# Kernel tuning notes

Measured on AMD Instinct MI355X. Metric: run time of the kernel, lower is better.

## Reference

```python
import jax, jax.numpy as jnp
import numpy as np
from jax import lax

B, T, BYTE_LEN, EMB = 8, 4096, 8, 64
FILTERS = [(1, 4), (2, 8), (3, 12), (4, 16), (5, 20), (6, 24), (7, 28)]
LAST_DIM = sum(c for _, c in FILTERS)  # 112
OUT_DIM = 512


def setup_inputs() -> dict:
    key = jax.random.key(0)
    ks = jax.random.split(key, 32)
    inp = {"features": jax.random.normal(ks[0], (B, T, BYTE_LEN, EMB), dtype=jnp.float32)}
    for i, (w, c) in enumerate(FILTERS):
        inp[f"conv_w{i+1}"] = jax.random.normal(ks[1 + i], (c, EMB, w), dtype=jnp.float32) * 0.05
        inp[f"conv_b{i+1}"] = jax.random.normal(ks[8 + i], (c,), dtype=jnp.float32) * 0.05
    inp["hw_w1"] = jax.random.normal(ks[15], (2 * LAST_DIM, LAST_DIM), dtype=jnp.float32) * 0.05
    inp["hw_b1"] = jnp.concatenate([jnp.zeros(LAST_DIM), jnp.ones(LAST_DIM)]).astype(jnp.float32)
    inp["hw_w2"] = jax.random.normal(ks[16], (2 * LAST_DIM, LAST_DIM), dtype=jnp.float32) * 0.05
    inp["hw_b2"] = jnp.concatenate([jnp.zeros(LAST_DIM), jnp.ones(LAST_DIM)]).astype(jnp.float32)
    inp["proj_w"] = jax.random.normal(ks[17], (OUT_DIM, LAST_DIM), dtype=jnp.float32) * 0.05
    inp["proj_b"] = jax.random.normal(ks[18], (OUT_DIM,), dtype=jnp.float32) * 0.05
    return inp


def _conv_branch(x, w, b):
    # x: [N, EMB, BYTE_LEN], w: [out_c, EMB, width] -> max over time, relu -> [N, out_c]
    y = lax.conv_general_dilated(x, w, window_strides=(1,), padding='VALID',
                                 dimension_numbers=('NCH', 'OIH', 'NCH'))
    y = y + b[None, :, None]
    return jax.nn.relu(jnp.max(y, axis=-1))


def _highway_layer(x, w, b):
    p = x @ w.T + b
    proj_x, gate = jnp.split(p, 2, axis=-1)
    g = jax.nn.sigmoid(gate)
    return g * x + (1.0 - g) * jax.nn.relu(proj_x)


def reference(features, conv_w1, conv_w2, conv_w3, conv_w4, conv_w5, conv_w6, conv_w7,
              conv_b1, conv_b2, conv_b3, conv_b4, conv_b5, conv_b6, conv_b7,
              hw_w1, hw_b1, hw_w2, hw_b2, proj_w, proj_b):
    b, t, byte_len, emb = features.shape
    # transpose(2,3).view(-1, emb, byte_len)
    x = features.transpose(0, 1, 3, 2).reshape(-1, emb, byte_len)  # [B*T, EMB, BYTE_LEN]
    ws = [conv_w1, conv_w2, conv_w3, conv_w4, conv_w5, conv_w6, conv_w7]
    bs = [conv_b1, conv_b2, conv_b3, conv_b4, conv_b5, conv_b6, conv_b7]
    branches = [_conv_branch(x, w, bb) for w, bb in zip(ws, bs)]
    h = jnp.concatenate(branches, axis=-1)  # [B*T, LAST_DIM]
    h = _highway_layer(h, hw_w1, hw_b1)
    h = _highway_layer(h, hw_w2, hw_b2)
    out = h @ proj_w.T + proj_b  # [B*T, OUT_DIM]
    return out.reshape(b, t, -1)
```

## Files before the change

### kernel.cpp

```cpp
#include <hip/hip_runtime.h>

typedef __attribute__((ext_vector_type(8))) short short8;
typedef __attribute__((ext_vector_type(4))) float f32x4;

#define KDIM 512
#define NCT  30
#define BCHUNK 32768

__device__ __forceinline__ unsigned short f2bf(float x) {
    unsigned u = __float_as_uint(x);
    return (unsigned short)((u + 0x7FFFu + ((u >> 16) & 1u)) >> 16);
}
__device__ __forceinline__ float bf2f(unsigned short h) {
    return __uint_as_float(((unsigned)h) << 16);
}

__device__ __forceinline__ void stage16(const void* g, void* l, int lane) {
    __builtin_amdgcn_global_load_lds(
        (const __attribute__((address_space(1))) unsigned int*)g,
        (__attribute__((address_space(3))) unsigned int*)l, 16, 0, 0);
}

__global__ __launch_bounds__(256) void prep_kernel(
        const float* __restrict__ w1, const float* __restrict__ w2,
        const float* __restrict__ w3, const float* __restrict__ w4,
        const float* __restrict__ w5, const float* __restrict__ w6,
        const float* __restrict__ w7, const float* __restrict__ hw1,
        const float* __restrict__ hw2, const float* __restrict__ pw,
        unsigned short* __restrict__ WC, unsigned short* __restrict__ W1s,
        unsigned short* __restrict__ W2s, unsigned short* __restrict__ Ps) {
    int gid = blockIdx.x * 256 + threadIdx.x;
    if (gid < 30720) {
        int kb = gid / 480, col = gid % 480;
        const float* wp; int cbnd, NP, C, W;
        if (col < 32)       { wp = w1; cbnd = 0;   NP = 8; C = 4;  W = 1; }
        else if (col < 96)  { wp = w2; cbnd = 32;  NP = 7; C = 8;  W = 2; }
        else if (col < 176) { wp = w3; cbnd = 96;  NP = 6; C = 12; W = 3; }
        else if (col < 256) { wp = w4; cbnd = 176; NP = 5; C = 16; W = 4; }
        else if (col < 336) { wp = w5; cbnd = 256; NP = 4; C = 20; W = 5; }
        else if (col < 416) { wp = w6; cbnd = 336; NP = 3; C = 24; W = 6; }
        else                { wp = w7; cbnd = 416; NP = 2; C = 28; W = 7; }
        int c2 = col - cbnd, oc = c2 / NP, p = c2 - oc * NP;
        int j = kb >> 3, dk = j - p, e0 = (kb & 7) * 8;
        bool valid = (oc < C) && (dk >= 0) && (dk < W);
        short8 v8;
#pragma unroll
        for (int i = 0; i < 8; ++i) {
            float v = valid ? wp[(oc * 64 + e0 + i) * W + dk] : 0.f;
            v8[i] = (short)f2bf(v);
        }
        int q = kb >> 2, krh = kb & 3;
        *(short8*)(WC + (size_t)q * 16384 + ((col >> 4) * 64 + krh * 16 + (col & 15)) * 8) = v8;
    } else if (gid < 30720 + 7168) {
        int x = gid - 30720;
        const float* src = (x < 3584) ? hw1 : hw2;
        unsigned short* dst = (x < 3584) ? W1s : W2s;
        if (x >= 3584) x -= 3584;
        int kb = x / 224, n = x % 224, k0 = kb * 8;
        short8 v8;
#pragma unroll
        for (int i = 0; i < 8; ++i) {
            float v = (k0 + i < 112) ? src[n * 112 + k0 + i] : 0.f;
            v8[i] = (short)f2bf(v);
        }
        int q = kb >> 2, krh = kb & 3;
        *(short8*)(dst + q * 8192 + ((n >> 4) * 64 + krh * 16 + (n & 15)) * 8) = v8;
    } else if (gid < 30720 + 7168 + 8192) {
        int x = gid - 37888;
        int kb = x / 512, n = x % 512, k0 = kb * 8;
        short8 v8;
#pragma unroll
        for (int i = 0; i < 8; ++i) {
            float v = (k0 + i < 112) ? pw[n * 112 + k0 + i] : 0.f;
            v8[i] = (short)f2bf(v);
        }
        int q = kb >> 2, krh = kb & 3;
        *(short8*)(Ps + ((q * 32 + (n >> 4)) * 64 + krh * 16 + (n & 15)) * 8) = v8;
    }
}

template <int T0, int NT>
__device__ __forceinline__ void dump_phase(float* Cb, const f32x4* acc, int wave, int lane) {
    int r0 = wave * 16 + ((lane >> 4) * 4);
    int c0 = lane & 15;
#pragma unroll
    for (int tt = 0; tt < NT; ++tt)
#pragma unroll
        for (int r = 0; r < 4; ++r)
            Cb[(r0 + r) * 161 + tt * 16 + c0] = acc[T0 + tt][r];
}

__device__ void reduce_phase(const float* Cb, unsigned short* ht, int tid,
                             int cA, int NPA, int choffA, int colbA, const float* cbA,
                             int cB, int NPB, int choffB, int colbB, const float* cbB) {
    int noc = cA + cB;
    for (int idx = tid; idx < 64 * noc; idx += 256) {
        int row = idx & 63, ocp = idx >> 6;
        bool isB = ocp >= cA;
        int oc = isB ? ocp - cA : ocp;
        int NP = isB ? NPB : NPA;
        int colb = isB ? colbB : colbA;
        int choff = isB ? choffB : choffA;
        const float* cb = isB ? cbB : cbA;
        const float* src = Cb + row * 161 + colb + oc * NP;
        float m = src[0];
        for (int k = 1; k < NP; ++k) m = fmaxf(m, src[k]);
        float v = fmaxf(m + cb[oc], 0.f);
        ht[row * 136 + choff + oc] = f2bf(v);
    }
}

__global__ __launch_bounds__(256, 2) void fused_kernel(
        const float* __restrict__ feat, const unsigned short* __restrict__ WC,
        const float* cb0, const float* cb1, const float* cb2, const float* cb3,
        const float* cb4, const float* cb5, const float* cb6,
        const unsigned short* __restrict__ W1, const unsigned short* __restrict__ W2,
        const unsigned short* __restrict__ PW,
        const float* __restrict__ hb1, const float* __restrict__ hb2,
        const float* __restrict__ pb, float* __restrict__ out) {
    __shared__ __align__(16) char sm[65536];
    const int tid = threadIdx.x, lane = tid & 63, wave = tid >> 6;
    const int c0 = lane & 15, kq = lane >> 4;
    const int m0 = blockIdx.x * 64;
    f32x4 zero = {0.f, 0.f, 0.f, 0.f};

    const float* arow = feat + (size_t)(m0 + wave * 16 + c0) * KDIM + kq * 8;
    short8 af[16];
#pragma unroll
    for (int q = 0; q < 16; ++q) {
        float t[8];
        *(float4*)(t)     = *(const float4*)(arow + q * 32);
        *(float4*)(t + 4) = *(const float4*)(arow + q * 32 + 4);
        short8 v;
#pragma unroll
        for (int i = 0; i < 8; ++i) v[i] = (short)f2bf(t[i]);
        af[q] = v;
    }

    f32x4 acc[NCT];
#pragma unroll
    for (int t = 0; t < NCT; ++t) acc[t] = zero;

    for (int i = tid; i < 2048; i += 256)
        stage16(WC + i * 8, sm + (i - lane) * 16, lane);

#pragma unroll
    for (int q = 0; q < 16; ++q) {
        if (q < 15) {
            const unsigned short* src = WC + (q + 1) * 16384;
            char* dst = sm + ((q + 1) & 1) * BCHUNK;
            for (int i = tid; i < 2048; i += 256)
                stage16(src + i * 8, dst + (i - lane) * 16, lane);
            asm volatile("s_waitcnt vmcnt(8)" ::: "memory");
        } else {
            asm volatile("s_waitcnt vmcnt(0)" ::: "memory");
        }
        __builtin_amdgcn_s_barrier();
        const char* bb = sm + (q & 1) * BCHUNK;
        __builtin_amdgcn_s_setprio(1);
#pragma unroll
        for (int t = 0; t < NCT; ++t) {
            short8 b = *(const short8*)(bb + (t * 64 + lane) * 16);
            acc[t] = __builtin_amdgcn_mfma_f32_16x16x32_bf16(af[q], b, acc[t], 0, 0, 0);
        }
        __builtin_amdgcn_s_setprio(0);
        asm volatile("s_waitcnt lgkmcnt(0)" ::: "memory");
        __builtin_amdgcn_s_barrier();
    }

    float* Cb = (float*)sm;
    unsigned short* ht = (unsigned short*)(sm + 41216);
    __syncthreads();
    for (int i = tid; i < 1024; i += 256)
        ht[(i >> 4) * 136 + 112 + (i & 15)] = 0;
    dump_phase<0, 6>(Cb, acc, wave, lane);
    __syncthreads();
    reduce_phase(Cb, ht, tid, 4, 8, 0, 0, cb0, 8, 7, 4, 32, cb1);
    __syncthreads();
    dump_phase<6, 10>(Cb, acc, wave, lane);
    __syncthreads();
    reduce_phase(Cb, ht, tid, 12, 6, 12, 0, cb2, 16, 5, 24, 80, cb3);
    __syncthreads();
    dump_phase<16, 10>(Cb, acc, wave, lane);
    __syncthreads();
    reduce_phase(Cb, ht, tid, 20, 4, 40, 0, cb4, 24, 3, 60, 80, cb5);
    __syncthreads();
    dump_phase<26, 4>(Cb, acc, wave, lane);
    __syncthreads();
    reduce_phase(Cb, ht, tid, 28, 2, 84, 0, cb6, 0, 1, 0, 0, cb6);
    __syncthreads();

    char* wb = sm;
    short8 a2[4];
#pragma unroll
    for (int q = 0; q < 4; ++q)
        a2[q] = *(const short8*)((const char*)ht + (wave * 16 + c0) * 272 + q * 64 + kq * 16);
    for (int i = tid; i < 1024; i += 256)
        stage16(W1 + i * 8, wb + (i - lane) * 16, lane);

    f32x4 acc2[14];
#pragma unroll
    for (int t = 0; t < 14; ++t) acc2[t] = zero;
#pragma unroll
    for (int q = 0; q < 4; ++q) {
        if (q < 3) {
            const unsigned short* src = W1 + (q + 1) * 8192;
            char* dst = wb + ((q + 1) & 1) * 16384;
            for (int i = tid; i < 1024; i += 256)
                stage16(src + i * 8, dst + (i - lane) * 16, lane);
        } else {
            for (int i = tid; i < 1024; i += 256)
                stage16(W2 + i * 8, wb + (i - lane) * 16, lane);
        }
        asm volatile("s_waitcnt vmcnt(4)" ::: "memory");
        __builtin_amdgcn_s_barrier();
        const char* bb = wb + (q & 1) * 16384;
#pragma unroll
        for (int t = 0; t < 14; ++t) {
            short8 b = *(const short8*)(bb + (t * 64 + lane) * 16);
            acc2[t] = __builtin_amdgcn_mfma_f32_16x16x32_bf16(a2[q], b, acc2[t], 0, 0, 0);
        }
        asm volatile("s_waitcnt lgkmcnt(0)" ::: "memory");
        __builtin_amdgcn_s_barrier();
    }

#pragma unroll
    for (int t = 0; t < 7; ++t) {
        float bp = hb1[t * 16 + c0], bg = hb1[112 + t * 16 + c0];
#pragma unroll
        for (int r = 0; r < 4; ++r) {
            int row = wave * 16 + kq * 4 + r;
            int col = t * 16 + c0;
            float px = acc2[t][r] + bp;
            float gt = acc2[t + 7][r] + bg;
            float g = 1.f / (1.f + __expf(-gt));
            float hres = bf2f(ht[row * 136 + col]);
            ht[row * 136 + col] = f2bf(g * hres + (1.f - g) * fmaxf(px, 0.f));
        }
    }

    short8 a3[4];
#pragma unroll
    for (int q = 0; q < 4; ++q)
        a3[q] = *(const short8*)((const char*)ht + (wave * 16 + c0) * 272 + q * 64 + kq * 16);

    f32x4 acc3[14];
#pragma unroll
    for (int t = 0; t < 14; ++t) acc3[t] = zero;
#pragma unroll
    for (int q = 0; q < 4; ++q) {
        if (q < 3) {
            const unsigned short* src = W2 + (q + 1) * 8192;
            char* dst = wb + ((q + 1) & 1) * 16384;
            for (int i = tid; i < 1024; i += 256)
                stage16(src + i * 8, dst + (i - lane) * 16, lane);
        } else {
            for (int i = tid; i < 1024; i += 256)
                stage16(PW + i * 8, wb + (i - lane) * 16, lane);
        }
        asm volatile("s_waitcnt vmcnt(4)" ::: "memory");
        __builtin_amdgcn_s_barrier();
        const char* bb = wb + (q & 1) * 16384;
#pragma unroll
        for (int t = 0; t < 14; ++t) {
            short8 b = *(const short8*)(bb + (t * 64 + lane) * 16);
            acc3[t] = __builtin_amdgcn_mfma_f32_16x16x32_bf16(a3[q], b, acc3[t], 0, 0, 0);
        }
        asm volatile("s_waitcnt lgkmcnt(0)" ::: "memory");
        __builtin_amdgcn_s_barrier();
    }

#pragma unroll
    for (int t = 0; t < 7; ++t) {
        float bp = hb2[t * 16 + c0], bg = hb2[112 + t * 16 + c0];
#pragma unroll
        for (int r = 0; r < 4; ++r) {
            int row = wave * 16 + kq * 4 + r;
            int col = t * 16 + c0;
            float px = acc3[t][r] + bp;
            float gt = acc3[t + 7][r] + bg;
            float g = 1.f / (1.f + __expf(-gt));
            float hres = bf2f(ht[row * 136 + col]);
            ht[row * 136 + col] = f2bf(g * hres + (1.f - g) * fmaxf(px, 0.f));
        }
    }

    short8 a4[4];
#pragma unroll
    for (int q = 0; q < 4; ++q)
        a4[q] = *(const short8*)((const char*)ht + (wave * 16 + c0) * 272 + q * 64 + kq * 16);

    char* pwb = sm;
    f32x4 acc4[32];
#pragma unroll
    for (int t = 0; t < 32; ++t) acc4[t] = zero;
#pragma unroll
    for (int c = 0; c < 8; ++c) {
        if (c < 7) {
            const unsigned short* src = PW + (c + 1) * 8192;
            char* dst = pwb + ((c + 1) & 1) * 16384;
            for (int i = tid; i < 1024; i += 256)
                stage16(src + i * 8, dst + (i - lane) * 16, lane);
            asm volatile("s_waitcnt vmcnt(4)" ::: "memory");
        } else {
            asm volatile("s_waitcnt vmcnt(0)" ::: "memory");
        }
        __builtin_amdgcn_s_barrier();
        const char* bb = pwb + (c & 1) * 16384;
        __builtin_amdgcn_s_setprio(1);
#pragma unroll
        for (int tt = 0; tt < 16; ++tt) {
            short8 b = *(const short8*)(bb + (tt * 64 + lane) * 16);
            acc4[(c & 1) * 16 + tt] =
                __builtin_amdgcn_mfma_f32_16x16x32_bf16(a4[c >> 1], b, acc4[(c & 1) * 16 + tt], 0, 0, 0);
        }
        __builtin_amdgcn_s_setprio(0);
        asm volatile("s_waitcnt lgkmcnt(0)" ::: "memory");
        __builtin_amdgcn_s_barrier();
    }

    float* ot = (float*)sm;
#pragma unroll
    for (int half = 0; half < 2; ++half) {
        __syncthreads();
#pragma unroll
        for (int t16 = 0; t16 < 16; ++t16) {
            int col = (half * 16 + t16) * 16 + c0;
            float b = pb[col];
#pragma unroll
            for (int r = 0; r < 4; ++r)
                ot[(wave * 16 + kq * 4 + r) * 256 + t16 * 16 + c0] = acc4[half * 16 + t16][r] + b;
        }
        __syncthreads();
        for (int i = tid; i < 4096; i += 256) {
            int row = i >> 6, c = i & 63;
            *(float4*)(out + (size_t)(m0 + row) * 512 + half * 256 + c * 4) = ((const float4*)ot)[i];
        }
    }
}

extern "C" void kernel_launch(void* const* d_in, const int* in_sizes, int n_in,
                              void* d_out, int out_size, void* d_ws, size_t ws_size,
                              hipStream_t stream) {
    const float* feat = (const float*)d_in[0];
    const float* cw[7];
    const float* cb[7];
    for (int f = 0; f < 7; ++f) {
        cw[f] = (const float*)d_in[1 + 2 * f];
        cb[f] = (const float*)d_in[2 + 2 * f];
    }
    const float* hw_w1 = (const float*)d_in[15];
    const float* hw_b1 = (const float*)d_in[16];
    const float* hw_w2 = (const float*)d_in[17];
    const float* hw_b2 = (const float*)d_in[18];
    const float* pw    = (const float*)d_in[19];
    const float* pb    = (const float*)d_in[20];
    float* out = (float*)d_out;

    char* ws = (char*)d_ws;
    unsigned short* WC  = (unsigned short*)ws;
    unsigned short* W1s = (unsigned short*)(ws + 524288);
    unsigned short* W2s = (unsigned short*)(ws + 589824);
    unsigned short* Ps  = (unsigned short*)(ws + 655360);

    prep_kernel<<<180, 256, 0, stream>>>(cw[0], cw[1], cw[2], cw[3], cw[4], cw[5], cw[6],
                                         hw_w1, hw_w2, pw, WC, W1s, W2s, Ps);
    fused_kernel<<<512, 256, 0, stream>>>(feat, WC, cb[0], cb[1], cb[2], cb[3], cb[4], cb[5], cb[6],
                                          W1s, W2s, Ps, hw_b1, hw_b2, pb, out);
}
```

Measured before the change: 192.7 us.

## Split fused kernel across 8 waves with column-group partitioning of MFMA tiles

The block grows from 4 to 8 waves. Each pair of waves shares a 16-row slice and splits the output column tiles, which halves the accumulators per wave (30→15 for conv, 14→8 for highway, 32→16 for projection). The feature A-fragments are now loaded and converted per K-chunk inside the main loop instead of all up front, and the prep kernel zero-pads extra weight tiles so the highway split is even. The aim is lower register pressure and more waves to hide memory latency, at the cost of duplicated A-fragment loads per wave pair and more barrier participants.

```diff
diff --git a/kernel.cpp b/kernel.cpp
--- a/kernel.cpp
+++ b/kernel.cpp
@@ -76,25 +76,36 @@
         }
         int q = kb >> 2, krh = kb & 3;
         *(short8*)(Ps + ((q * 32 + (n >> 4)) * 64 + krh * 16 + (n & 15)) * 8) = v8;
+    } else if (gid < 30720 + 7168 + 8192 + 1024) {
+        int x = gid - 46080;
+        unsigned short* dst = (x < 512) ? W1s : W2s;
+        x &= 511;
+        int q = x >> 7, tt = 14 + ((x >> 6) & 1), e = x & 63;
+        short8 z = {0, 0, 0, 0, 0, 0, 0, 0};
+        *(short8*)(dst + q * 8192 + tt * 512 + e * 8) = z;
     }
 }
 
 template <int T0, int NT>
-__device__ __forceinline__ void dump_phase(float* Cb, const f32x4* acc, int wave, int lane) {
-    int r0 = wave * 16 + ((lane >> 4) * 4);
+__device__ __forceinline__ void dump_phase(float* Cb, const f32x4* acc, int cg, int rg, int lane) {
+    int r0 = rg * 16 + ((lane >> 4) * 4);
     int c0 = lane & 15;
 #pragma unroll
-    for (int tt = 0; tt < NT; ++tt)
-#pragma unroll
-        for (int r = 0; r < 4; ++r)
-            Cb[(r0 + r) * 161 + tt * 16 + c0] = acc[T0 + tt][r];
+    for (int tt = 0; tt < NT; ++tt) {
+        const int gt = T0 + tt;
+        if ((gt / 15) == cg) {
+#pragma unroll
+            for (int r = 0; r < 4; ++r)
+                Cb[(r0 + r) * 161 + tt * 16 + c0] = acc[gt % 15][r];
+        }
+    }
 }
 
 __device__ void reduce_phase(const float* Cb, unsigned short* ht, int tid,
                              int cA, int NPA, int choffA, int colbA, const float* cbA,
                              int cB, int NPB, int choffB, int colbB, const float* cbB) {
     int noc = cA + cB;
-    for (int idx = tid; idx < 64 * noc; idx += 256) {
+    for (int idx = tid; idx < 64 * noc; idx += 512) {
         int row = idx & 63, ocp = idx >> 6;
         bool isB = ocp >= cA;
         int oc = isB ? ocp - cA : ocp;
@@ -110,7 +121,7 @@
     }
 }
 
-__global__ __launch_bounds__(256, 2) void fused_kernel(
+__global__ __launch_bounds__(512, 4) void fused_kernel(
         const float* __restrict__ feat, const unsigned short* __restrict__ WC,
         const float* cb0, const float* cb1, const float* cb2, const float* cb3,
         const float* cb4, const float* cb5, const float* cb6,
@@ -120,48 +131,44 @@
         const float* __restrict__ pb, float* __restrict__ out) {
     __shared__ __align__(16) char sm[65536];
     const int tid = threadIdx.x, lane = tid & 63, wave = tid >> 6;
+    const int rg = wave >> 1, cg = wave & 1;
     const int c0 = lane & 15, kq = lane >> 4;
     const int m0 = blockIdx.x * 64;
     f32x4 zero = {0.f, 0.f, 0.f, 0.f};
 
-    const float* arow = feat + (size_t)(m0 + wave * 16 + c0) * KDIM + kq * 8;
-    short8 af[16];
+    const float* arow = feat + (size_t)(m0 + rg * 16 + c0) * KDIM + kq * 8;
+    f32x4 acc[15];
+#pragma unroll
+    for (int t = 0; t < 15; ++t) acc[t] = zero;
+    const int cgoff = cg * 15 * 1024;
+
+    for (int i = tid; i < 2048; i += 512)
+        stage16(WC + i * 8, sm + (i - lane) * 16, lane);
+
 #pragma unroll
     for (int q = 0; q < 16; ++q) {
-        float t[8];
-        *(float4*)(t)     = *(const float4*)(arow + q * 32);
-        *(float4*)(t + 4) = *(const float4*)(arow + q * 32 + 4);
-        short8 v;
-#pragma unroll
-        for (int i = 0; i < 8; ++i) v[i] = (short)f2bf(t[i]);
-        af[q] = v;
-    }
-
-    f32x4 acc[NCT];
-#pragma unroll
-    for (int t = 0; t < NCT; ++t) acc[t] = zero;
-
-    for (int i = tid; i < 2048; i += 256)
-        stage16(WC + i * 8, sm + (i - lane) * 16, lane);
-
-#pragma unroll
-    for (int q = 0; q < 16; ++q) {
+        float t0[4], t1[4];
+        *(float4*)(t0) = *(const float4*)(arow + q * 32);
+        *(float4*)(t1) = *(const float4*)(arow + q * 32 + 4);
         if (q < 15) {
             const unsigned short* src = WC + (q + 1) * 16384;
             char* dst = sm + ((q + 1) & 1) * BCHUNK;
-            for (int i = tid; i < 2048; i += 256)
+            for (int i = tid; i < 2048; i += 512)
                 stage16(src + i * 8, dst + (i - lane) * 16, lane);
-            asm volatile("s_waitcnt vmcnt(8)" ::: "memory");
+            asm volatile("s_waitcnt vmcnt(4)" ::: "memory");
         } else {
             asm volatile("s_waitcnt vmcnt(0)" ::: "memory");
         }
         __builtin_amdgcn_s_barrier();
-        const char* bb = sm + (q & 1) * BCHUNK;
+        short8 a;
+#pragma unroll
+        for (int i = 0; i < 4; ++i) { a[i] = (short)f2bf(t0[i]); a[4 + i] = (short)f2bf(t1[i]); }
+        const char* bb = sm + (q & 1) * BCHUNK + cgoff;
         __builtin_amdgcn_s_setprio(1);
 #pragma unroll
-        for (int t = 0; t < NCT; ++t) {
-            short8 b = *(const short8*)(bb + (t * 64 + lane) * 16);
-            acc[t] = __builtin_amdgcn_mfma_f32_16x16x32_bf16(af[q], b, acc[t], 0, 0, 0);
+        for (int t = 0; t < 15; ++t) {
+            short8 b = *(const short8*)(bb + t * 1024 + lane * 16);
+            acc[t] = __builtin_amdgcn_mfma_f32_16x16x32_bf16(a, b, acc[t], 0, 0, 0);
         }
         __builtin_amdgcn_s_setprio(0);
         asm volatile("s_waitcnt lgkmcnt(0)" ::: "memory");
@@ -170,138 +177,163 @@
 
     float* Cb = (float*)sm;
     unsigned short* ht = (unsigned short*)(sm + 41216);
-    __syncthreads();
-    for (int i = tid; i < 1024; i += 256)
+    for (int i = tid; i < 1024; i += 512)
         ht[(i >> 4) * 136 + 112 + (i & 15)] = 0;
-    dump_phase<0, 6>(Cb, acc, wave, lane);
-    __syncthreads();
+    dump_phase<0, 6>(Cb, acc, cg, rg, lane);
+    asm volatile("s_waitcnt lgkmcnt(0)" ::: "memory");
+    __builtin_amdgcn_s_barrier();
     reduce_phase(Cb, ht, tid, 4, 8, 0, 0, cb0, 8, 7, 4, 32, cb1);
-    __syncthreads();
-    dump_phase<6, 10>(Cb, acc, wave, lane);
-    __syncthreads();
+    asm volatile("s_waitcnt lgkmcnt(0)" ::: "memory");
+    __builtin_amdgcn_s_barrier();
+    dump_phase<6, 10>(Cb, acc, cg, rg, lane);
+    asm volatile("s_waitcnt lgkmcnt(0)" ::: "memory");
+    __builtin_amdgcn_s_barrier();
     reduce_phase(Cb, ht, tid, 12, 6, 12, 0, cb2, 16, 5, 24, 80, cb3);
-    __syncthreads();
-    dump_phase<16, 10>(Cb, acc, wave, lane);
-    __syncthreads();
+    asm volatile("s_waitcnt lgkmcnt(0)" ::: "memory");
+    __builtin_amdgcn_s_barrier();
+    dump_phase<16, 10>(Cb, acc, cg, rg, lane);
+    asm volatile("s_waitcnt lgkmcnt(0)" ::: "memory");
+    __builtin_amdgcn_s_barrier();
     reduce_phase(Cb, ht, tid, 20, 4, 40, 0, cb4, 24, 3, 60, 80, cb5);
-    __syncthreads();
-    dump_phase<26, 4>(Cb, acc, wave, lane);
-    __syncthreads();
+    asm volatile("s_waitcnt lgkmcnt(0)" ::: "memory");
+    __builtin_amdgcn_s_barrier();
+    dump_phase<26, 4>(Cb, acc, cg, rg, lane);
+    asm volatile("s_waitcnt lgkmcnt(0)" ::: "memory");
+    __builtin_amdgcn_s_barrier();
     reduce_phase(Cb, ht, tid, 28, 2, 84, 0, cb6, 0, 1, 0, 0, cb6);
-    __syncthreads();
+    asm volatile("s_waitcnt lgkmcnt(0)" ::: "memory");
+    __builtin_amdgcn_s_barrier();
 
     char* wb = sm;
     short8 a2[4];
 #pragma unroll
     for (int q = 0; q < 4; ++q)
-        a2[q] = *(const short8*)((const char*)ht + (wave * 16 + c0) * 272 + q * 64 + kq * 16);
-    for (int i = tid; i < 1024; i += 256)
+        a2[q] = *(const short8*)((const char*)ht + (rg * 16 + c0) * 272 + q * 64 + kq * 16);
+    for (int i = tid; i < 1024; i += 512)
         stage16(W1 + i * 8, wb + (i - lane) * 16, lane);
 
-    f32x4 acc2[14];
-#pragma unroll
-    for (int t = 0; t < 14; ++t) acc2[t] = zero;
+    f32x4 p2[4], g2[4];
+#pragma unroll
+    for (int j = 0; j < 4; ++j) { p2[j] = zero; g2[j] = zero; }
 #pragma unroll
     for (int q = 0; q < 4; ++q) {
         if (q < 3) {
             const unsigned short* src = W1 + (q + 1) * 8192;
             char* dst = wb + ((q + 1) & 1) * 16384;
-            for (int i = tid; i < 1024; i += 256)
+            for (int i = tid; i < 1024; i += 512)
                 stage16(src + i * 8, dst + (i - lane) * 16, lane);
         } else {
-            for (int i = tid; i < 1024; i += 256)
+            for (int i = tid; i < 1024; i += 512)
                 stage16(W2 + i * 8, wb + (i - lane) * 16, lane);
         }
-        asm volatile("s_waitcnt vmcnt(4)" ::: "memory");
+        asm volatile("s_waitcnt vmcnt(2)" ::: "memory");
         __builtin_amdgcn_s_barrier();
         const char* bb = wb + (q & 1) * 16384;
 #pragma unroll
-        for (int t = 0; t < 14; ++t) {
-            short8 b = *(const short8*)(bb + (t * 64 + lane) * 16);
-            acc2[t] = __builtin_amdgcn_mfma_f32_16x16x32_bf16(a2[q], b, acc2[t], 0, 0, 0);
+        for (int j = 0; j < 4; ++j) {
+            int pt = (cg == 0) ? j : ((j < 3) ? 4 + j : 14);
+            int gt = (pt == 14) ? 15 : pt + 7;
+            short8 bp = *(const short8*)(bb + pt * 1024 + lane * 16);
+            short8 bg = *(const short8*)(bb + gt * 1024 + lane * 16);
+            p2[j] = __builtin_amdgcn_mfma_f32_16x16x32_bf16(a2[q], bp, p2[j], 0, 0, 0);
+            g2[j] = __builtin_amdgcn_mfma_f32_16x16x32_bf16(a2[q], bg, g2[j], 0, 0, 0);
         }
         asm volatile("s_waitcnt lgkmcnt(0)" ::: "memory");
         __builtin_amdgcn_s_barrier();
     }
 
 #pragma unroll
-    for (int t = 0; t < 7; ++t) {
-        float bp = hb1[t * 16 + c0], bg = hb1[112 + t * 16 + c0];
-#pragma unroll
-        for (int r = 0; r < 4; ++r) {
-            int row = wave * 16 + kq * 4 + r;
-            int col = t * 16 + c0;
-            float px = acc2[t][r] + bp;
-            float gt = acc2[t + 7][r] + bg;
-            float g = 1.f / (1.f + __expf(-gt));
-            float hres = bf2f(ht[row * 136 + col]);
-            ht[row * 136 + col] = f2bf(g * hres + (1.f - g) * fmaxf(px, 0.f));
-        }
-    }
+    for (int j = 0; j < 4; ++j) {
+        int pt = (cg == 0) ? j : ((j < 3) ? 4 + j : 14);
+        if (pt < 7) {
+            float bp = hb1[pt * 16 + c0], bg = hb1[112 + pt * 16 + c0];
+#pragma unroll
+            for (int r = 0; r < 4; ++r) {
+                int row = rg * 16 + kq * 4 + r;
+                int col = pt * 16 + c0;
+                float px = p2[j][r] + bp;
+                float gv = g2[j][r] + bg;
+                float g = 1.f / (1.f + __expf(-gv));
+                float hres = bf2f(ht[row * 136 + col]);
+                ht[row * 136 + col] = f2bf(g * hres + (1.f - g) * fmaxf(px, 0.f));
+            }
+        }
+    }
+    asm volatile("s_waitcnt lgkmcnt(0)" ::: "memory");
+    __builtin_amdgcn_s_barrier();
 
     short8 a3[4];
 #pragma unroll
     for (int q = 0; q < 4; ++q)
-        a3[q] = *(const short8*)((const char*)ht + (wave * 16 + c0) * 272 + q * 64 + kq * 16);
-
-    f32x4 acc3[14];
-#pragma unroll
-    for (int t = 0; t < 14; ++t) acc3[t] = zero;
+        a3[q] = *(const short8*)((const char*)ht + (rg * 16 + c0) * 272 + q * 64 + kq * 16);
+
+    f32x4 p3[4], g3[4];
+#pragma unroll
+    for (int j = 0; j < 4; ++j) { p3[j] = zero; g3[j] = zero; }
 #pragma unroll
     for (int q = 0; q < 4; ++q) {
         if (q < 3) {
             const unsigned short* src = W2 + (q + 1) * 8192;
             char* dst = wb + ((q + 1) & 1) * 16384;
-            for (int i = tid; i < 1024; i += 256)
+            for (int i = tid; i < 1024; i += 512)
                 stage16(src + i * 8, dst + (i - lane) * 16, lane);
         } else {
-            for (int i = tid; i < 1024; i += 256)
+            for (int i = tid; i < 1024; i += 512)
                 stage16(PW + i * 8, wb + (i - lane) * 16, lane);
         }
-        asm volatile("s_waitcnt vmcnt(4)" ::: "memory");
+        asm volatile("s_waitcnt vmcnt(2)" ::: "memory");
         __builtin_amdgcn_s_barrier();
         const char* bb = wb + (q & 1) * 16384;
 #pragma unroll
-        for (int t = 0; t < 14; ++t) {
-            short8 b = *(const short8*)(bb + (t * 64 + lane) * 16);
-            acc3[t] = __builtin_amdgcn_mfma_f32_16x16x32_bf16(a3[q], b, acc3[t], 0, 0, 0);
+        for (int j = 0; j < 4; ++j) {
+            int pt = (cg == 0) ? j : ((j < 3) ? 4 + j : 14);
+            int gt = (pt == 14) ? 15 : pt + 7;
+            short8 bp = *(const short8*)(bb + pt * 1024 + lane * 16);
+            short8 bg = *(const short8*)(bb + gt * 1024 + lane * 16);
+            p3[j] = __builtin_amdgcn_mfma_f32_16x16x32_bf16(a3[q], bp, p3[j], 0, 0, 0);
+            g3[j] = __builtin_amdgcn_mfma_f32_16x16x32_bf16(a3[q], bg, g3[j], 0, 0, 0);
         }
         asm volatile("s_waitcnt lgkmcnt(0)" ::: "memory");
         __builtin_amdgcn_s_barrier();
     }
 
 #pragma unroll
-    for (int t = 0; t < 7; ++t) {
-        float bp = hb2[t * 16 + c0], bg = hb2[112 + t * 16 + c0];
-#pragma unroll
-        for (int r = 0; r < 4; ++r) {
-            int row = wave * 16 + kq * 4 + r;
-            int col = t * 16 + c0;
-            float px = acc3[t][r] + bp;
-            float gt = acc3[t + 7][r] + bg;
-            float g = 1.f / (1.f + __expf(-gt));
-            float hres = bf2f(ht[row * 136 + col]);
-            ht[row * 136 + col] = f2bf(g * hres + (1.f - g) * fmaxf(px, 0.f));
-        }
-    }
+    for (int j = 0; j < 4; ++j) {
+        int pt = (cg == 0) ? j : ((j < 3) ? 4 + j : 14);
+        if (pt < 7) {
+            float bp = hb2[pt * 16 + c0], bg = hb2[112 + pt * 16 + c0];
+#pragma unroll
+            for (int r = 0; r < 4; ++r) {
+                int row = rg * 16 + kq * 4 + r;
+                int col = pt * 16 + c0;
+                float px = p3[j][r] + bp;
+                float gv = g3[j][r] + bg;
+                float g = 1.f / (1.f + __expf(-gv));
+                float hres = bf2f(ht[row * 136 + col]);
+                ht[row * 136 + col] = f2bf(g * hres + (1.f - g) * fmaxf(px, 0.f));
+            }
+        }
+    }
+    asm volatile("s_waitcnt lgkmcnt(0)" ::: "memory");
+    __builtin_amdgcn_s_barrier();
 
     short8 a4[4];
 #pragma unroll
     for (int q = 0; q < 4; ++q)
-        a4[q] = *(const short8*)((const char*)ht + (wave * 16 + c0) * 272 + q * 64 + kq * 16);
+        a4[q] = *(const short8*)((const char*)ht + (rg * 16 + c0) * 272 + q * 64 + kq * 16);
 
     char* pwb = sm;
-    f32x4 acc4[32];
-#pragma unroll
-    for (int t = 0; t < 32; ++t) acc4[t] = zero;
+    f32x4 acc4[16];
+#pragma unroll
+    for (int t = 0; t < 16; ++t) acc4[t] = zero;
 #pragma unroll
     for (int c = 0; c < 8; ++c) {
         if (c < 7) {
             const unsigned short* src = PW + (c + 1) * 8192;
             char* dst = pwb + ((c + 1) & 1) * 16384;
-            for (int i = tid; i < 1024; i += 256)
+            for (int i = tid; i < 1024; i += 512)
                 stage16(src + i * 8, dst + (i - lane) * 16, lane);
-            asm volatile("s_waitcnt vmcnt(4)" ::: "memory");
+            asm volatile("s_waitcnt vmcnt(2)" ::: "memory");
         } else {
             asm volatile("s_waitcnt vmcnt(0)" ::: "memory");
         }
@@ -309,10 +341,11 @@
         const char* bb = pwb + (c & 1) * 16384;
         __builtin_amdgcn_s_setprio(1);
 #pragma unroll
-        for (int tt = 0; tt < 16; ++tt) {
-            short8 b = *(const short8*)(bb + (tt * 64 + lane) * 16);
-            acc4[(c & 1) * 16 + tt] =
-                __builtin_amdgcn_mfma_f32_16x16x32_bf16(a4[c >> 1], b, acc4[(c & 1) * 16 + tt], 0, 0, 0);
+        for (int j = 0; j < 8; ++j) {
+            int tt = cg * 8 + j;
+            short8 b = *(const short8*)(bb + tt * 1024 + lane * 16);
+            int ai = (c & 1) * 8 + j;
+            acc4[ai] = __builtin_amdgcn_mfma_f32_16x16x32_bf16(a4[c >> 1], b, acc4[ai], 0, 0, 0);
         }
         __builtin_amdgcn_s_setprio(0);
         asm volatile("s_waitcnt lgkmcnt(0)" ::: "memory");
@@ -321,20 +354,21 @@
 
     float* ot = (float*)sm;
 #pragma unroll
-    for (int half = 0; half < 2; ++half) {
+    for (int h = 0; h < 2; ++h) {
         __syncthreads();
 #pragma unroll
-        for (int t16 = 0; t16 < 16; ++t16) {
-            int col = (half * 16 + t16) * 16 + c0;
+        for (int j = 0; j < 8; ++j) {
+            int tt = cg * 8 + j;
+            int col = (h * 16 + tt) * 16 + c0;
             float b = pb[col];
 #pragma unroll
             for (int r = 0; r < 4; ++r)
-                ot[(wave * 16 + kq * 4 + r) * 256 + t16 * 16 + c0] = acc4[half * 16 + t16][r] + b;
+                ot[(rg * 16 + kq * 4 + r) * 256 + tt * 16 + c0] = acc4[h * 8 + j][r] + b;
         }
         __syncthreads();
-        for (int i = tid; i < 4096; i += 256) {
-            int row = i >> 6, c = i & 63;
-            *(float4*)(out + (size_t)(m0 + row) * 512 + half * 256 + c * 4) = ((const float4*)ot)[i];
+        for (int i = tid; i < 4096; i += 512) {
+            int row = i >> 6, cc = i & 63;
+            *(float4*)(out + (size_t)(m0 + row) * 512 + h * 256 + cc * 4) = ((const float4*)ot)[i];
         }
     }
 }
@@ -363,8 +397,8 @@
     unsigned short* W2s = (unsigned short*)(ws + 589824);
     unsigned short* Ps  = (unsigned short*)(ws + 655360);
 
-    prep_kernel<<<180, 256, 0, stream>>>(cw[0], cw[1], cw[2], cw[3], cw[4], cw[5], cw[6],
+    prep_kernel<<<184, 256, 0, stream>>>(cw[0], cw[1], cw[2], cw[3], cw[4], cw[5], cw[6],
                                          hw_w1, hw_w2, pw, WC, W1s, W2s, Ps);
-    fused_kernel<<<512, 256, 0, stream>>>(feat, WC, cb[0], cb[1], cb[2], cb[3], cb[4], cb[5], cb[6],
+    fused_kernel<<<512, 512, 0, stream>>>(feat, WC, cb[0], cb[1], cb[2], cb[3], cb[4], cb[5], cb[6],
                                           W1s, W2s, Ps, hw_b1, hw_b2, pb, out);
 }
```

Measured after the change: 189.4 us. No clear change (-1.7%).
